# Kernel optimization log

Hardware: AMD Instinct MI355X
Metric: run time of the kernel (lower is better)

The kernel has to match this reference:

```python
import jax, jax.numpy as jnp
import numpy as np

NUM_HEADS = 32
HEAD_DIM = 128
HIDDEN = 4096
MAX_SEQ = 4096
B, S = 8, 16
POS = 2048


def setup_inputs() -> dict:
    key = jax.random.key(0)
    ks = jax.random.split(key, 7)
    sc = 1.0 / np.sqrt(HIDDEN)
    return {
        "h": jax.random.normal(ks[0], (B, S, HIDDEN), dtype=jnp.float32),
        "Wq": jax.random.normal(ks[1], (HIDDEN, HIDDEN), dtype=jnp.float32) * sc,
        "Wk": jax.random.normal(ks[2], (HIDDEN, HIDDEN), dtype=jnp.float32) * sc,
        "Wv": jax.random.normal(ks[3], (HIDDEN, HIDDEN), dtype=jnp.float32) * sc,
        "Wo": jax.random.normal(ks[4], (HIDDEN, HIDDEN), dtype=jnp.float32) * sc,
        "K_cache": jax.random.normal(ks[5], (B, NUM_HEADS, MAX_SEQ, HEAD_DIM), dtype=jnp.float32),
        "V_cache": jax.random.normal(ks[6], (B, NUM_HEADS, MAX_SEQ, HEAD_DIM), dtype=jnp.float32),
        "pos": POS,
    }


def reference(h, Wq, Wk, Wv, Wo, K_cache, V_cache, pos):
    b, s, _ = h.shape
    # QKV projections (Linear with weight [out, in], no bias): h @ W.T
    def proj(W):
        return (h @ W.T).reshape(b, s, NUM_HEADS, HEAD_DIM).transpose(0, 2, 1, 3)  # [B,H,S,hd]
    Q, K, V = proj(Wq), proj(Wk), proj(Wv)
    # write new K/V into cache at [pos : pos+S] (pos is a static Python int)
    K_cache = K_cache.at[:, :, pos:pos + s, :].set(K)
    V_cache = V_cache.at[:, :, pos:pos + s, :].set(V)
    K_all = K_cache[:, :, :pos + s, :]  # [B,H,T,hd], T = pos+S
    V_all = V_cache[:, :, :pos + s, :]
    scores = jnp.einsum('bhsd,bhtd->bhst', Q, K_all) / np.sqrt(HEAD_DIM)  # [B,H,S,T]
    if s > 1:
        # causal mask applied only to the freshly-written block of columns
        causal = jnp.triu(jnp.full((s, s), -jnp.inf, dtype=scores.dtype), k=1)
        scores = scores.at[:, :, :, pos:pos + s].add(causal)
    attn = jax.nn.softmax(scores, axis=-1)
    out = jnp.einsum('bhst,bhtd->bhsd', attn, V_all)  # [B,H,S,hd]
    out = out.transpose(0, 2, 1, 3).reshape(b, s, NUM_HEADS * HEAD_DIM)
    return out @ Wo.T
```

## Files before the change

### kernel.cpp

```cpp
#include <hip/hip_runtime.h>

typedef _Float16 f16;
typedef _Float16 f16x8 __attribute__((ext_vector_type(8)));
typedef _Float16 f16x4 __attribute__((ext_vector_type(4)));
typedef _Float16 f16x2 __attribute__((ext_vector_type(2)));
typedef float f32x4 __attribute__((ext_vector_type(4)));
typedef float f32x2 __attribute__((ext_vector_type(2)));

#define MFMA16(a, b, c) __builtin_amdgcn_mfma_f32_16x16x32_f16(a, b, c, 0, 0, 0)

#define HID 4096
#define ROWS 128
#define SCL 0.12751743f

__device__ __forceinline__ f16x8 cvt8(float4 x, float4 y) {
    f16x8 v = {(f16)x.x, (f16)x.y, (f16)x.z, (f16)x.w,
               (f16)y.x, (f16)y.y, (f16)y.z, (f16)y.w};
    return v;
}

__device__ __forceinline__ int swz2(int row, int cb) {
    return row * 256 + (cb ^ ((row & 7) << 4));
}

__global__ void k_cvt(const float* __restrict__ src, f16* __restrict__ dst) {
    const int i = blockIdx.x * blockDim.x + threadIdx.x;
    const float4* s4 = (const float4*)src + (size_t)i * 2;
    float4 x = s4[0], y = s4[1];
    *((f16x8*)dst + i) = cvt8(x, y);
}

__global__ __launch_bounds__(256) void k_proj(
        const f16* __restrict__ hb,
        const float* __restrict__ Wq, const float* __restrict__ Wk,
        const float* __restrict__ Wv,
        f16* __restrict__ Qw, f16* __restrict__ Kw, f16* __restrict__ Vw) {
    const int mat = blockIdx.x >> 8;
    const int ct  = blockIdx.x & 255;
    const float* __restrict__ W = (mat == 0) ? Wq : (mat == 1) ? Wk : Wv;
    f16* __restrict__ Ob = (mat == 0) ? Qw : (mat == 1) ? Kw : Vw;
    const int c0 = ct * 16;

    __shared__ __align__(16) f16 sA[128 * 128];
    __shared__ __align__(16) f16 sB[16 * 128];

    const int tid = threadIdx.x;
    const int w = tid >> 6, l = tid & 63;
    const int rw = w * 32;
    const int ar = tid >> 4;
    const int ac = (tid & 15) * 8;

    f32x4 acc0 = {}, acc1 = {};

    float4 wx, wy;
    f16x8 hreg[8];
    {
        const float* wp = W + (size_t)(c0 + ar) * HID + ac;
        wx = *(const float4*)wp; wy = *(const float4*)(wp + 4);
        #pragma unroll
        for (int c = 0; c < 8; ++c)
            hreg[c] = *(const f16x8*)(hb + (size_t)(c * 16 + ar) * HID + ac);
    }

    for (int ks = 0; ks < 32; ++ks) {
        #pragma unroll
        for (int c = 0; c < 8; ++c)
            *(f16x8*)((char*)sA + swz2(c * 16 + ar, ac * 2)) = hreg[c];
        *(f16x8*)((char*)sB + swz2(ar, ac * 2)) = cvt8(wx, wy);
        __syncthreads();
        if (ks < 31) {
            const int k0 = (ks + 1) * 128;
            const float* wp = W + (size_t)(c0 + ar) * HID + k0 + ac;
            wx = *(const float4*)wp; wy = *(const float4*)(wp + 4);
            #pragma unroll
            for (int c = 0; c < 8; ++c)
                hreg[c] = *(const f16x8*)(hb + (size_t)(c * 16 + ar) * HID + k0 + ac);
        }
        #pragma unroll
        for (int kk = 0; kk < 4; ++kk) {
            const int cb = kk * 64 + (l >> 4) * 16;
            f16x8 a0 = *(const f16x8*)((char*)sA + swz2(rw + (l & 15), cb));
            f16x8 a1 = *(const f16x8*)((char*)sA + swz2(rw + 16 + (l & 15), cb));
            f16x8 b0 = *(const f16x8*)((char*)sB + swz2((l & 15), cb));
            acc0 = MFMA16(a0, b0, acc0);
            acc1 = MFMA16(a1, b0, acc1);
        }
        __syncthreads();
    }
    #pragma unroll
    for (int r = 0; r < 4; ++r) {
        const int col = c0 + (l & 15);
        Ob[(size_t)(rw + (l >> 4) * 4 + r) * HID + col]      = (f16)acc0[r];
        Ob[(size_t)(rw + 16 + (l >> 4) * 4 + r) * HID + col] = (f16)acc1[r];
    }
}

__global__ __launch_bounds__(512) void k_attn(
        const f16* __restrict__ Qw, const f16* __restrict__ Kw,
        const f16* __restrict__ Vw,
        const float* __restrict__ Kc, const float* __restrict__ Vc,
        const int* __restrict__ posp, f16* __restrict__ Ow) {

    __shared__ __align__(16) char smem[65536 + 1024];

    const int bh = blockIdx.x;
    const int b = bh >> 5, hh = bh & 31;
    const int tid = threadIdx.x, w = tid >> 6, l = tid & 63;
    const int pos = *posp;
    const int npure = pos >> 5;

    const float* Kb = Kc + (size_t)bh * (4096 * 128);
    const float* Vb = Vc + (size_t)bh * (4096 * 128);

    f16x8 qf[4];
    {
        const f16* qp = Qw + (size_t)(b * 16 + (l & 15)) * HID + hh * 128 + (l >> 4) * 8;
        #pragma unroll
        for (int kk = 0; kk < 4; ++kk) qf[kk] = *(const f16x8*)(qp + kk * 32);
    }

    f32x4 o[8] = {};
    float m[4], lsum[4];
    #pragma unroll
    for (int r = 0; r < 4; ++r) { m[r] = -3e38f; lsum[r] = 0.f; }

    f16* Pw = (f16*)smem + w * 640;

    const int start = (w * npure) >> 3;
    const int end   = ((w + 1) * npure) >> 3;
    for (int tau = start; tau < end; ++tau) {
        const int t0 = tau << 5;

        f16x8 kf[2][4];
        #pragma unroll
        for (int tn = 0; tn < 2; ++tn) {
            const float* kp = Kb + (size_t)(t0 + tn * 16 + (l & 15)) * 128 + (l >> 4) * 8;
            #pragma unroll
            for (int kk = 0; kk < 4; ++kk) {
                float4 x = *(const float4*)(kp + kk * 32);
                float4 y = *(const float4*)(kp + kk * 32 + 4);
                kf[tn][kk] = cvt8(x, y);
            }
        }
        f32x4 sa[2] = {};
        #pragma unroll
        for (int tn = 0; tn < 2; ++tn)
            #pragma unroll
            for (int kk = 0; kk < 4; ++kk) sa[tn] = MFMA16(qf[kk], kf[tn][kk], sa[tn]);

        f16x8 vf[8];
        {
            const float* vp = Vb + (size_t)(t0 + (l >> 4) * 8) * 128 + (l & 15);
            #pragma unroll
            for (int dt = 0; dt < 8; ++dt)
                #pragma unroll
                for (int j = 0; j < 8; ++j) vf[dt][j] = (f16)vp[j * 128 + dt * 16];
        }

        float sc[2][4];
        #pragma unroll
        for (int tn = 0; tn < 2; ++tn)
            #pragma unroll
            for (int r = 0; r < 4; ++r) sc[tn][r] = sa[tn][r] * SCL;
        float vmax[4];
        #pragma unroll
        for (int r = 0; r < 4; ++r) vmax[r] = fmaxf(sc[0][r], sc[1][r]);
        #pragma unroll
        for (int d = 1; d < 16; d <<= 1)
            #pragma unroll
            for (int r = 0; r < 4; ++r) vmax[r] = fmaxf(vmax[r], __shfl_xor(vmax[r], d));
        float p[2][4], rs[4], fac[4];
        #pragma unroll
        for (int r = 0; r < 4; ++r) {
            const float mn = fmaxf(m[r], vmax[r]);
            fac[r] = exp2f(m[r] - mn);
            m[r] = mn;
            p[0][r] = exp2f(sc[0][r] - mn);
            p[1][r] = exp2f(sc[1][r] - mn);
            rs[r] = p[0][r] + p[1][r];
            lsum[r] *= fac[r];
        }
        #pragma unroll
        for (int d = 1; d < 16; d <<= 1)
            #pragma unroll
            for (int r = 0; r < 4; ++r) rs[r] += __shfl_xor(rs[r], d);
        #pragma unroll
        for (int r = 0; r < 4; ++r) lsum[r] += rs[r];
        #pragma unroll
        for (int dt = 0; dt < 8; ++dt)
            #pragma unroll
            for (int r = 0; r < 4; ++r) o[dt][r] *= fac[r];

        #pragma unroll
        for (int r = 0; r < 4; ++r) {
            const int s_ = (l >> 4) * 4 + r;
            Pw[s_ * 40 + (l & 15)]      = (f16)p[0][r];
            Pw[s_ * 40 + 16 + (l & 15)] = (f16)p[1][r];
        }
        asm volatile("s_waitcnt lgkmcnt(0)" ::: "memory");
        f16x8 pa = *(const f16x8*)(Pw + (l & 15) * 40 + (l >> 4) * 8);

        #pragma unroll
        for (int dt = 0; dt < 8; ++dt) o[dt] = MFMA16(pa, vf[dt], o[dt]);
    }

    if (w == 7) {
        for (int t0 = npure << 5; t0 < pos + 16; t0 += 32) {
            f32x4 sa[2] = {};
            bool tnv[2];
            #pragma unroll
            for (int tn = 0; tn < 2; ++tn) {
                tnv[tn] = (t0 + tn * 16 < pos + 16);
                if (!tnv[tn]) continue;
                const int trow = t0 + tn * 16 + (l & 15);
                f16x8 kf[4];
                if (trow < pos) {
                    const float* kp = Kb + (size_t)trow * 128 + (l >> 4) * 8;
                    #pragma unroll
                    for (int kk = 0; kk < 4; ++kk) {
                        float4 x = *(const float4*)(kp + kk * 32);
                        float4 y = *(const float4*)(kp + kk * 32 + 4);
                        kf[kk] = cvt8(x, y);
                    }
                } else {
                    const int tt = trow - pos;
                    const int rr = tt < 15 ? tt : 15;
                    const f16* kp = Kw + (size_t)(b * 16 + rr) * HID + hh * 128 + (l >> 4) * 8;
                    #pragma unroll
                    for (int kk = 0; kk < 4; ++kk) kf[kk] = *(const f16x8*)(kp + kk * 32);
                }
                #pragma unroll
                for (int kk = 0; kk < 4; ++kk) sa[tn] = MFMA16(qf[kk], kf[kk], sa[tn]);
            }

            float sc[2][4];
            #pragma unroll
            for (int tn = 0; tn < 2; ++tn) {
                const int tg = t0 + tn * 16 + (l & 15);
                #pragma unroll
                for (int r = 0; r < 4; ++r) {
                    if (!tnv[tn]) { sc[tn][r] = -3e38f; continue; }
                    float v = sa[tn][r] * SCL;
                    if (tg >= pos) {
                        const int tt = tg - pos;
                        const int s_ = (l >> 4) * 4 + r;
                        if (tt > s_ || tt >= 16) v = -3e38f;
                    }
                    sc[tn][r] = v;
                }
            }

            float vmax[4];
            #pragma unroll
            for (int r = 0; r < 4; ++r) vmax[r] = fmaxf(sc[0][r], sc[1][r]);
            #pragma unroll
            for (int d = 1; d < 16; d <<= 1)
                #pragma unroll
                for (int r = 0; r < 4; ++r) vmax[r] = fmaxf(vmax[r], __shfl_xor(vmax[r], d));
            float p[2][4], rs[4], fac[4];
            #pragma unroll
            for (int r = 0; r < 4; ++r) {
                const float mn = fmaxf(m[r], vmax[r]);
                fac[r] = exp2f(m[r] - mn);
                m[r] = mn;
                p[0][r] = sc[0][r] < -1e29f ? 0.f : exp2f(sc[0][r] - mn);
                p[1][r] = sc[1][r] < -1e29f ? 0.f : exp2f(sc[1][r] - mn);
                rs[r] = p[0][r] + p[1][r];
                lsum[r] *= fac[r];
            }
            #pragma unroll
            for (int d = 1; d < 16; d <<= 1)
                #pragma unroll
                for (int r = 0; r < 4; ++r) rs[r] += __shfl_xor(rs[r], d);
            #pragma unroll
            for (int r = 0; r < 4; ++r) lsum[r] += rs[r];
            #pragma unroll
            for (int dt = 0; dt < 8; ++dt)
                #pragma unroll
                for (int r = 0; r < 4; ++r) o[dt][r] *= fac[r];

            #pragma unroll
            for (int r = 0; r < 4; ++r) {
                const int s_ = (l >> 4) * 4 + r;
                Pw[s_ * 40 + (l & 15)]      = (f16)p[0][r];
                Pw[s_ * 40 + 16 + (l & 15)] = (f16)p[1][r];
            }
            asm volatile("s_waitcnt lgkmcnt(0)" ::: "memory");
            f16x8 pa = *(const f16x8*)(Pw + (l & 15) * 40 + (l >> 4) * 8);

            const int tb = t0 + (l >> 4) * 8;
            #pragma unroll
            for (int dt = 0; dt < 8; ++dt) {
                f16x8 vf;
                #pragma unroll
                for (int j = 0; j < 8; ++j) {
                    const int t = tb + j;
                    if (t < pos) {
                        vf[j] = (f16)Vb[(size_t)t * 128 + dt * 16 + (l & 15)];
                    } else {
                        const int rr = (t - pos < 15) ? (t - pos) : 15;
                        vf[j] = Vw[(size_t)(b * 16 + rr) * HID + hh * 128 + dt * 16 + (l & 15)];
                    }
                }
                o[dt] = MFMA16(pa, vf, o[dt]);
            }
        }
    }

    __syncthreads();
    float* Osh = (float*)smem;
    float* Msh = (float*)(smem + 65536);
    float* Lsh = Msh + 128;
    #pragma unroll
    for (int dt = 0; dt < 8; ++dt)
        #pragma unroll
        for (int r = 0; r < 4; ++r)
            Osh[w * 2048 + ((l >> 4) * 4 + r) * 128 + dt * 16 + (l & 15)] = o[dt][r];
    if ((l & 15) == 0) {
        #pragma unroll
        for (int r = 0; r < 4; ++r) {
            Msh[w * 16 + (l >> 4) * 4 + r] = m[r];
            Lsh[w * 16 + (l >> 4) * 4 + r] = lsum[r];
        }
    }
    __syncthreads();
    {
        const int s_ = tid >> 5;
        const int d_ = (tid & 31) * 4;
        float M = -3e38f;
        #pragma unroll
        for (int ww = 0; ww < 8; ++ww) M = fmaxf(M, Msh[ww * 16 + s_]);
        float L = 0.f;
        f32x4 oa = {};
        #pragma unroll
        for (int ww = 0; ww < 8; ++ww) {
            const float e = exp2f(Msh[ww * 16 + s_] - M);
            L += e * Lsh[ww * 16 + s_];
            f32x4 v = *(const f32x4*)(Osh + ww * 2048 + s_ * 128 + d_);
            #pragma unroll
            for (int r = 0; r < 4; ++r) oa[r] += e * v[r];
        }
        const float inv = 1.f / L;
        f16x4 res = {(f16)(oa[0] * inv), (f16)(oa[1] * inv),
                     (f16)(oa[2] * inv), (f16)(oa[3] * inv)};
        *(f16x4*)(Ow + (size_t)(b * 16 + s_) * HID + hh * 128 + d_) = res;
    }
}

__global__ __launch_bounds__(256) void k_oproj(
        const f16* __restrict__ Oa, const float* __restrict__ Wo,
        float* __restrict__ out) {
    const int c0 = blockIdx.x * 16;

    __shared__ __align__(16) f16 sA[128 * 128];
    __shared__ __align__(16) f16 sB[16 * 128];

    const int tid = threadIdx.x;
    const int w = tid >> 6, l = tid & 63;
    const int rw = w * 32;
    const int ar = tid >> 4;
    const int ac = (tid & 15) * 8;

    f32x4 acc0 = {}, acc1 = {};

    float4 wx, wy;
    f16x8 hreg[8];
    {
        const float* wp = Wo + (size_t)(c0 + ar) * HID + ac;
        wx = *(const float4*)wp; wy = *(const float4*)(wp + 4);
        #pragma unroll
        for (int c = 0; c < 8; ++c)
            hreg[c] = *(const f16x8*)(Oa + (size_t)(c * 16 + ar) * HID + ac);
    }

    for (int ks = 0; ks < 32; ++ks) {
        #pragma unroll
        for (int c = 0; c < 8; ++c)
            *(f16x8*)((char*)sA + swz2(c * 16 + ar, ac * 2)) = hreg[c];
        *(f16x8*)((char*)sB + swz2(ar, ac * 2)) = cvt8(wx, wy);
        __syncthreads();
        if (ks < 31) {
            const int k0 = (ks + 1) * 128;
            const float* wp = Wo + (size_t)(c0 + ar) * HID + k0 + ac;
            wx = *(const float4*)wp; wy = *(const float4*)(wp + 4);
            #pragma unroll
            for (int c = 0; c < 8; ++c)
                hreg[c] = *(const f16x8*)(Oa + (size_t)(c * 16 + ar) * HID + k0 + ac);
        }
        #pragma unroll
        for (int kk = 0; kk < 4; ++kk) {
            const int cb = kk * 64 + (l >> 4) * 16;
            f16x8 a0 = *(const f16x8*)((char*)sA + swz2(rw + (l & 15), cb));
            f16x8 a1 = *(const f16x8*)((char*)sA + swz2(rw + 16 + (l & 15), cb));
            f16x8 b0 = *(const f16x8*)((char*)sB + swz2((l & 15), cb));
            acc0 = MFMA16(a0, b0, acc0);
            acc1 = MFMA16(a1, b0, acc1);
        }
        __syncthreads();
    }
    #pragma unroll
    for (int r = 0; r < 4; ++r) {
        const int col = c0 + (l & 15);
        out[(size_t)(rw + (l >> 4) * 4 + r) * HID + col]      = acc0[r];
        out[(size_t)(rw + 16 + (l >> 4) * 4 + r) * HID + col] = acc1[r];
    }
}

extern "C" void kernel_launch(void* const* d_in, const int* in_sizes, int n_in,
                              void* d_out, int out_size, void* d_ws, size_t ws_size,
                              hipStream_t stream) {
    const float* h  = (const float*)d_in[0];
    const float* Wq = (const float*)d_in[1];
    const float* Wk = (const float*)d_in[2];
    const float* Wv = (const float*)d_in[3];
    const float* Wo = (const float*)d_in[4];
    const float* Kc = (const float*)d_in[5];
    const float* Vc = (const float*)d_in[6];
    const int* pos  = (const int*)d_in[7];
    float* out = (float*)d_out;

    f16* hws = (f16*)d_ws;
    f16* Qw  = hws + ROWS * HID;
    f16* Kw  = Qw + ROWS * HID;
    f16* Vw  = Kw + ROWS * HID;
    f16* Ow  = Vw + ROWS * HID;

    k_cvt<<<256, 256, 0, stream>>>(h, hws);
    k_proj<<<768, 256, 0, stream>>>(hws, Wq, Wk, Wv, Qw, Kw, Vw);
    k_attn<<<256, 512, 0, stream>>>(Qw, Kw, Vw, Kc, Vc, pos, Ow);
    k_oproj<<<256, 256, 0, stream>>>(Ow, Wo, out);
}
```

Measured before the change: 205.6 us.

## Double-buffer weight tile and deepen prefetch in projection GEMMs via shared core

```diff
diff --git a/kernel.cpp b/kernel.cpp
--- a/kernel.cpp
+++ b/kernel.cpp
@@ -3,9 +3,7 @@
 typedef _Float16 f16;
 typedef _Float16 f16x8 __attribute__((ext_vector_type(8)));
 typedef _Float16 f16x4 __attribute__((ext_vector_type(4)));
-typedef _Float16 f16x2 __attribute__((ext_vector_type(2)));
 typedef float f32x4 __attribute__((ext_vector_type(4)));
-typedef float f32x2 __attribute__((ext_vector_type(2)));
 
 #define MFMA16(a, b, c) __builtin_amdgcn_mfma_f32_16x16x32_f16(a, b, c, 0, 0, 0)
 
@@ -28,6 +26,73 @@
     const float4* s4 = (const float4*)src + (size_t)i * 2;
     float4 x = s4[0], y = s4[1];
     *((f16x8*)dst + i) = cvt8(x, y);
+}
+
+__device__ __forceinline__ void gemm_core(
+        const f16* __restrict__ Ab, const float* __restrict__ W,
+        int c0, int tid, f16* __restrict__ sA, f16* __restrict__ sB,
+        f32x4& acc0, f32x4& acc1) {
+    const int w = tid >> 6, l = tid & 63;
+    const int rw = w * 32;
+    const int ar = tid >> 4;
+    const int ac = (tid & 15) * 8;
+
+    const float* wrow = W + (size_t)(c0 + ar) * HID + ac;
+    const f16*   arow = Ab + (size_t)ar * HID + ac;
+
+    float4 wx, wy, wnx = {}, wny = {};
+
+    {
+        float4 w0x = *(const float4*)wrow;
+        float4 w0y = *(const float4*)(wrow + 4);
+        *(f16x8*)((char*)sB + swz2(ar, ac * 2)) = cvt8(w0x, w0y);
+        #pragma unroll
+        for (int c = 0; c < 8; ++c) {
+            f16x8 hv = *(const f16x8*)(arow + (size_t)c * 16 * HID);
+            *(f16x8*)((char*)sA + swz2(c * 16 + ar, ac * 2)) = hv;
+        }
+        wx = *(const float4*)(wrow + 128);
+        wy = *(const float4*)(wrow + 128 + 4);
+    }
+    asm volatile("s_waitcnt lgkmcnt(0)" ::: "memory");
+    __builtin_amdgcn_sched_barrier(0);
+    __builtin_amdgcn_s_barrier();
+
+    for (int ks = 0; ks < 32; ++ks) {
+        const int buf = ks & 1;
+        f16x8 Hn[8];
+        if (ks < 31) {
+            const int kh = (ks + 1) * 128;
+            #pragma unroll
+            for (int c = 0; c < 8; ++c)
+                Hn[c] = *(const f16x8*)(arow + (size_t)c * 16 * HID + kh);
+            if (ks < 30) {
+                const float* wp = wrow + (ks + 2) * 128;
+                wnx = *(const float4*)wp; wny = *(const float4*)(wp + 4);
+            }
+            *(f16x8*)((char*)sB + (buf ^ 1) * 4096 + swz2(ar, ac * 2)) = cvt8(wx, wy);
+        }
+        #pragma unroll
+        for (int kk = 0; kk < 4; ++kk) {
+            const int cb = kk * 64 + (l >> 4) * 16;
+            f16x8 a0 = *(const f16x8*)((char*)sA + swz2(rw + (l & 15), cb));
+            f16x8 a1 = *(const f16x8*)((char*)sA + swz2(rw + 16 + (l & 15), cb));
+            f16x8 b0 = *(const f16x8*)((char*)sB + buf * 4096 + swz2((l & 15), cb));
+            acc0 = MFMA16(a0, b0, acc0);
+            acc1 = MFMA16(a1, b0, acc1);
+        }
+        if (ks < 31) {
+            __builtin_amdgcn_sched_barrier(0);
+            __builtin_amdgcn_s_barrier();
+            #pragma unroll
+            for (int c = 0; c < 8; ++c)
+                *(f16x8*)((char*)sA + swz2(c * 16 + ar, ac * 2)) = Hn[c];
+            wx = wnx; wy = wny;
+            asm volatile("s_waitcnt lgkmcnt(0)" ::: "memory");
+            __builtin_amdgcn_sched_barrier(0);
+            __builtin_amdgcn_s_barrier();
+        }
+    }
 }
 
 __global__ __launch_bounds__(256) void k_proj(
@@ -42,56 +107,43 @@
     const int c0 = ct * 16;
 
     __shared__ __align__(16) f16 sA[128 * 128];
-    __shared__ __align__(16) f16 sB[16 * 128];
+    __shared__ __align__(16) f16 sB[2 * 16 * 128];
 
     const int tid = threadIdx.x;
     const int w = tid >> 6, l = tid & 63;
-    const int rw = w * 32;
-    const int ar = tid >> 4;
-    const int ac = (tid & 15) * 8;
 
     f32x4 acc0 = {}, acc1 = {};
-
-    float4 wx, wy;
-    f16x8 hreg[8];
-    {
-        const float* wp = W + (size_t)(c0 + ar) * HID + ac;
-        wx = *(const float4*)wp; wy = *(const float4*)(wp + 4);
-        #pragma unroll
-        for (int c = 0; c < 8; ++c)
-            hreg[c] = *(const f16x8*)(hb + (size_t)(c * 16 + ar) * HID + ac);
-    }
-
-    for (int ks = 0; ks < 32; ++ks) {
-        #pragma unroll
-        for (int c = 0; c < 8; ++c)
-            *(f16x8*)((char*)sA + swz2(c * 16 + ar, ac * 2)) = hreg[c];
-        *(f16x8*)((char*)sB + swz2(ar, ac * 2)) = cvt8(wx, wy);
-        __syncthreads();
-        if (ks < 31) {
-            const int k0 = (ks + 1) * 128;
-            const float* wp = W + (size_t)(c0 + ar) * HID + k0 + ac;
-            wx = *(const float4*)wp; wy = *(const float4*)(wp + 4);
-            #pragma unroll
-            for (int c = 0; c < 8; ++c)
-                hreg[c] = *(const f16x8*)(hb + (size_t)(c * 16 + ar) * HID + k0 + ac);
-        }
-        #pragma unroll
-        for (int kk = 0; kk < 4; ++kk) {
-            const int cb = kk * 64 + (l >> 4) * 16;
-            f16x8 a0 = *(const f16x8*)((char*)sA + swz2(rw + (l & 15), cb));
-            f16x8 a1 = *(const f16x8*)((char*)sA + swz2(rw + 16 + (l & 15), cb));
-            f16x8 b0 = *(const f16x8*)((char*)sB + swz2((l & 15), cb));
-            acc0 = MFMA16(a0, b0, acc0);
-            acc1 = MFMA16(a1, b0, acc1);
-        }
-        __syncthreads();
-    }
+    gemm_core(hb, W, c0, tid, sA, sB, acc0, acc1);
+
     #pragma unroll
     for (int r = 0; r < 4; ++r) {
+        const int row = w * 32 + (l >> 4) * 4 + r;
         const int col = c0 + (l & 15);
-        Ob[(size_t)(rw + (l >> 4) * 4 + r) * HID + col]      = (f16)acc0[r];
-        Ob[(size_t)(rw + 16 + (l >> 4) * 4 + r) * HID + col] = (f16)acc1[r];
+        Ob[(size_t)row * HID + col]        = (f16)acc0[r];
+        Ob[(size_t)(row + 16) * HID + col] = (f16)acc1[r];
+    }
+}
+
+__global__ __launch_bounds__(256) void k_oproj(
+        const f16* __restrict__ Oa, const float* __restrict__ Wo,
+        float* __restrict__ out) {
+    const int c0 = blockIdx.x * 16;
+
+    __shared__ __align__(16) f16 sA[128 * 128];
+    __shared__ __align__(16) f16 sB[2 * 16 * 128];
+
+    const int tid = threadIdx.x;
+    const int w = tid >> 6, l = tid & 63;
+
+    f32x4 acc0 = {}, acc1 = {};
+    gemm_core(Oa, Wo, c0, tid, sA, sB, acc0, acc1);
+
+    #pragma unroll
+    for (int r = 0; r < 4; ++r) {
+        const int row = w * 32 + (l >> 4) * 4 + r;
+        const int col = c0 + (l & 15);
+        out[(size_t)row * HID + col]        = acc0[r];
+        out[(size_t)(row + 16) * HID + col] = acc1[r];
     }
 }
 
@@ -347,65 +399,6 @@
     }
 }
 
-__global__ __launch_bounds__(256) void k_oproj(
-        const f16* __restrict__ Oa, const float* __restrict__ Wo,
-        float* __restrict__ out) {
-    const int c0 = blockIdx.x * 16;
-
-    __shared__ __align__(16) f16 sA[128 * 128];
-    __shared__ __align__(16) f16 sB[16 * 128];
-
-    const int tid = threadIdx.x;
-    const int w = tid >> 6, l = tid & 63;
-    const int rw = w * 32;
-    const int ar = tid >> 4;
-    const int ac = (tid & 15) * 8;
-
-    f32x4 acc0 = {}, acc1 = {};
-
-    float4 wx, wy;
-    f16x8 hreg[8];
-    {
-        const float* wp = Wo + (size_t)(c0 + ar) * HID + ac;
-        wx = *(const float4*)wp; wy = *(const float4*)(wp + 4);
-        #pragma unroll
-        for (int c = 0; c < 8; ++c)
-            hreg[c] = *(const f16x8*)(Oa + (size_t)(c * 16 + ar) * HID + ac);
-    }
-
-    for (int ks = 0; ks < 32; ++ks) {
-        #pragma unroll
-        for (int c = 0; c < 8; ++c)
-            *(f16x8*)((char*)sA + swz2(c * 16 + ar, ac * 2)) = hreg[c];
-        *(f16x8*)((char*)sB + swz2(ar, ac * 2)) = cvt8(wx, wy);
-        __syncthreads();
-        if (ks < 31) {
-            const int k0 = (ks + 1) * 128;
-            const float* wp = Wo + (size_t)(c0 + ar) * HID + k0 + ac;
-            wx = *(const float4*)wp; wy = *(const float4*)(wp + 4);
-            #pragma unroll
-            for (int c = 0; c < 8; ++c)
-                hreg[c] = *(const f16x8*)(Oa + (size_t)(c * 16 + ar) * HID + k0 + ac);
-        }
-        #pragma unroll
-        for (int kk = 0; kk < 4; ++kk) {
-            const int cb = kk * 64 + (l >> 4) * 16;
-            f16x8 a0 = *(const f16x8*)((char*)sA + swz2(rw + (l & 15), cb));
-            f16x8 a1 = *(const f16x8*)((char*)sA + swz2(rw + 16 + (l & 15), cb));
-            f16x8 b0 = *(const f16x8*)((char*)sB + swz2((l & 15), cb));
-            acc0 = MFMA16(a0, b0, acc0);
-            acc1 = MFMA16(a1, b0, acc1);
-        }
-        __syncthreads();
-    }
-    #pragma unroll
-    for (int r = 0; r < 4; ++r) {
-        const int col = c0 + (l & 15);
-        out[(size_t)(rw + (l >> 4) * 4 + r) * HID + col]      = acc0[r];
-        out[(size_t)(rw + 16 + (l >> 4) * 4 + r) * HID + col] = acc1[r];
-    }
-}
-
 extern "C" void kernel_launch(void* const* d_in, const int* in_sizes, int n_in,
                               void* d_out, int out_size, void* d_ws, size_t ws_size,
                               hipStream_t stream) {
```

Measured after the change: 208.6 us. Within noise of the previous version (+1.5%).
